# Kernel tuning notes

Measured on AMD Instinct MI355X. Metric: run time of the kernel, lower is better.

The kernel has to match this reference:

```python
import jax, jax.numpy as jnp
import numpy as np

N_NODES = 20000
N_EDGES = 320000
N_GRAPHS = 64
IN_DIM = 768
HID = 256
HEADS = 4
NUM_CLASSES = 5
NEG_SLOPE = 0.2  # PyG GATConv default leaky_relu slope


def setup_inputs() -> dict:
    key = jax.random.key(0)
    ks = jax.random.split(key, 20)
    x = jax.random.normal(ks[0], (N_NODES, IN_DIM), dtype=jnp.float32)
    edge_index = jax.random.randint(ks[1], (2, N_EDGES), 0, N_NODES, dtype=jnp.int32)
    batch = jnp.sort(jax.random.randint(ks[2], (N_NODES,), 0, N_GRAPHS, dtype=jnp.int32))
    s = lambda k, sh: jax.random.normal(k, sh, dtype=jnp.float32) * (1.0 / np.sqrt(sh[0]))
    HC = HEADS * HID
    return {
        "x": x, "edge_index": edge_index, "batch": batch,
        "Wp": s(ks[3], (IN_DIM, HID)), "bp": jnp.zeros((HID,), jnp.float32),
        "W1": s(ks[4], (HID, HC)),
        "as1": jax.random.normal(ks[5], (HEADS, HID)) * 0.1,
        "ad1": jax.random.normal(ks[6], (HEADS, HID)) * 0.1,
        "b1": jnp.zeros((HC,), jnp.float32),
        "W2": s(ks[7], (HC, HC)),
        "as2": jax.random.normal(ks[8], (HEADS, HID)) * 0.1,
        "ad2": jax.random.normal(ks[9], (HEADS, HID)) * 0.1,
        "b2": jnp.zeros((HC,), jnp.float32),
        "Wc1": s(ks[10], (2 * HC, 256)), "bc1": jnp.zeros((256,), jnp.float32),
        "Wc2": s(ks[11], (256, NUM_CLASSES)), "bc2": jnp.zeros((NUM_CLASSES,), jnp.float32),
    }


def _gat(h, src, dst, W, att_s, att_d, bias):
    # PyG GATConv (concat=True), dropout in eval mode (identity).
    N = h.shape[0]
    hW = (h @ W).reshape(N, HEADS, HID)             # [N,H,C]
    a_s = jnp.einsum('nhc,hc->nh', hW, att_s)        # per-node src score
    a_d = jnp.einsum('nhc,hc->nh', hW, att_d)
    e = jax.nn.leaky_relu(a_s[src] + a_d[dst], NEG_SLOPE)  # [E,H]
    # segment softmax over incoming edges of each destination node
    m = jax.ops.segment_max(e, dst, num_segments=N)
    e = jnp.exp(e - m[dst])
    denom = jax.ops.segment_sum(e, dst, num_segments=N)
    alpha = e / (denom[dst] + 1e-16)
    msg = hW[src] * alpha[:, :, None]                # [E,H,C]
    out = jax.ops.segment_sum(msg, dst, num_segments=N)
    return out.reshape(N, HEADS * HID) + bias


def reference(x, edge_index, batch, Wp, bp, W1, as1, ad1, b1, W2, as2, ad2, b2, Wc1, bc1, Wc2, bc2):
    N = x.shape[0]
    # add self-loops (PyG GATConv default add_self_loops=True)
    loop = jnp.arange(N, dtype=edge_index.dtype)
    src = jnp.concatenate([edge_index[0], loop])
    dst = jnp.concatenate([edge_index[1], loop])

    h = jax.nn.relu(x @ Wp + bp)
    h = jax.nn.elu(_gat(h, src, dst, W1, as1, ad1, b1))
    h = jax.nn.elu(_gat(h, src, dst, W2, as2, ad2, b2))

    # global mean / max pool over graphs
    cnt = jax.ops.segment_sum(jnp.ones((N,), h.dtype), batch, num_segments=N_GRAPHS)
    mean_pool = jax.ops.segment_sum(h, batch, num_segments=N_GRAPHS) / jnp.maximum(cnt, 1.0)[:, None]
    max_pool = jax.ops.segment_max(h, batch, num_segments=N_GRAPHS)
    g = jnp.concatenate([mean_pool, max_pool], axis=1)  # [G, 2*H*C]

    hcls = jax.nn.relu(g @ Wc1 + bc1)
    return hcls @ Wc2 + bc2
```

## Files before the change

### kernel.cpp

```cpp
#include <hip/hip_runtime.h>
#include <hip/hip_fp16.h>
#include <math.h>

#define N_HID 256
#define N_HEADS 4
#define N_HC 1024
#define N_GRAPHS 64

typedef __attribute__((ext_vector_type(4))) float f32x4;
typedef _Float16 half8 __attribute__((ext_vector_type(8)));
typedef _Float16 half4 __attribute__((ext_vector_type(4)));

__device__ __forceinline__ void gl_lds16h(const __half* g, __half* l) {
    __builtin_amdgcn_global_load_lds(
        (const __attribute__((address_space(1))) unsigned int*)g,
        (__attribute__((address_space(3))) unsigned int*)l, 16, 0, 0);
}

__global__ __launch_bounds__(256) void k_deg(const int* __restrict__ dst, int E,
                                             int* __restrict__ deg) {
    int e = blockIdx.x * 256 + threadIdx.x;
    if (e < E) atomicAdd(&deg[dst[e]], 1);
}

__global__ __launch_bounds__(1024) void k_scan(const int* __restrict__ deg,
                                               int* __restrict__ rowstart, int N) {
    __shared__ int part[1024];
    const int t = threadIdx.x;
    const int chunk = (N + 1023) / 1024;
    const int c0 = t * chunk;
    int s = 0;
    for (int i = 0; i < chunk; i++) {
        int idx = c0 + i;
        if (idx < N) s += deg[idx];
    }
    part[t] = s;
    __syncthreads();
    for (int off = 1; off < 1024; off <<= 1) {
        int v = (t >= off) ? part[t - off] : 0;
        __syncthreads();
        part[t] += v;
        __syncthreads();
    }
    int run = (t == 0) ? 0 : part[t - 1];
    if (t == 0) rowstart[0] = 0;
    for (int i = 0; i < chunk; i++) {
        int idx = c0 + i;
        if (idx < N) {
            run += deg[idx];
            rowstart[idx + 1] = run;
        }
    }
}

__global__ __launch_bounds__(256) void k_fill(const int* __restrict__ src,
                                              const int* __restrict__ dst, int E,
                                              const int* __restrict__ rowstart,
                                              int* __restrict__ cursor,
                                              int* __restrict__ col) {
    int e = blockIdx.x * 256 + threadIdx.x;
    if (e < E) {
        int d = dst[e];
        int p = atomicAdd(&cursor[d], 1);
        col[rowstart[d] + p] = src[e];
    }
}

__global__ __launch_bounds__(256) void k_wtt(const float* __restrict__ W,
                                             __half* __restrict__ WT, int K, int N) {
    __shared__ float tile[32][33];
    const int k0 = blockIdx.y * 32, n0 = blockIdx.x * 32;
    const int tr = threadIdx.x >> 5, tc = threadIdx.x & 31;
#pragma unroll
    for (int rr = 0; rr < 4; rr++) {
        int k = k0 + tr + rr * 8;
        tile[tr + rr * 8][tc] = W[(size_t)k * N + n0 + tc];
    }
    __syncthreads();
#pragma unroll
    for (int rr = 0; rr < 4; rr++) {
        int n = n0 + tr + rr * 8;
        WT[(size_t)n * K + k0 + tc] = __float2half(tile[tc][tr + rr * 8]);
    }
}

__global__ __launch_bounds__(256) void k_makeva(const __half* __restrict__ W1T,
                                                const float* __restrict__ as1,
                                                const float* __restrict__ ad1,
                                                float* __restrict__ va) {
    __shared__ float satt[256];
    int b = blockIdx.x;
    int h = b & 3, isd = b >> 2;
    int k = threadIdx.x;
    const float* att = (isd ? ad1 : as1) + h * 256;
    satt[k] = att[k];
    __syncthreads();
    const __half* wr = W1T + (size_t)(h * 256) * 256 + k;
    float s = 0.f;
    for (int c = 0; c < 256; c++) s += __half2float(wr[(size_t)c * 256]) * satt[c];
    va[b * 256 + k] = s;
}

__global__ __launch_bounds__(256) void k_makeva2(const __half* __restrict__ W2T,
                                                 const float* __restrict__ as2,
                                                 const float* __restrict__ ad2,
                                                 float* __restrict__ va2) {
    __shared__ float satt[32];
    int b = blockIdx.x;
    int h = b & 3;
    int jc = blockIdx.y;
    int t = threadIdx.x;
    const float* att = (b >= 4 ? ad2 : as2) + h * 256 + jc * 32;
    if (t < 32) satt[t] = att[t];
    __syncthreads();
    float s0 = 0.f, s1 = 0.f, s2 = 0.f, s3 = 0.f;
    const __half* base = W2T + (size_t)(h * 256 + jc * 32) * 1024 + t * 4;
    for (int j = 0; j < 32; j++) {
        half4 wv = *reinterpret_cast<const half4*>(base + (size_t)j * 1024);
        float a = satt[j];
        s0 += a * (float)wv[0]; s1 += a * (float)wv[1];
        s2 += a * (float)wv[2]; s3 += a * (float)wv[3];
    }
    float* o = va2 + b * 1024 + t * 4;
    atomicAdd(o + 0, s0); atomicAdd(o + 1, s1);
    atomicAdd(o + 2, s2); atomicAdd(o + 3, s3);
}

template <int EPI, int COSCHED>
__global__ __launch_bounds__(256) void k_gemm2p(
    const __half* __restrict__ A, const __half* __restrict__ BT,
    const float* __restrict__ bias, __half* __restrict__ C,
    int M, int NROW, int K, int lda, int ldc,
    int aoffz, int boffz, int coffz, int bofz) {
    __shared__ __half sA[2][128 * 32];
    __shared__ __half sB[2][128 * 32];
    int bm, bn;
    size_t coff = 0;
    if (COSCHED) {
        const int bid = blockIdx.x;
        const int xcd = bid & 7, j0 = bid >> 3;
        const int br = xcd + 8 * (j0 >> 3);
        const int bc = j0 & 7;
        if (br >= NROW) return;
        bm = br * 128; bn = bc * 128;
    } else {
        const int z = blockIdx.z;
        A += (size_t)z * aoffz;
        BT += (size_t)z * boffz;
        bias += z * bofz;
        coff = (size_t)z * coffz;
        bm = blockIdx.y * 128; bn = blockIdx.x * 128;
    }
    const int tid = threadIdx.x, lane = tid & 63, w = tid >> 6;
    const int wr = (w >> 1) * 64, wc = (w & 1) * 64;
    const bool isB = (w >= 2);
    const __half* gsrc = isB ? (BT + (size_t)bn * K) : (A + (size_t)bm * lda);
    const int gld = isB ? K : lda;
    const int rbase = (w & 1) * 64;
    const int lr = lane >> 2, lsl = lane & 3;
    const int g = lane >> 4, fr = lane & 15;
    const int nt = K >> 5;

    f32x4 acc[4][4] = {};

    auto STAGE = [&](int b, int t) {
        __half* sbuf = (isB ? sB[b] : sA[b]);
        const int k0 = t << 5;
#pragma unroll
        for (int c2 = 0; c2 < 4; c2++) {
            int row = rbase + c2 * 16 + lr;
            int slg = lsl ^ ((row >> 1) & 3);
            gl_lds16h(gsrc + (size_t)row * gld + k0 + slg * 8,
                      sbuf + (rbase + c2 * 16) * 32);
        }
    };

    STAGE(0, 0);
    int cur = 0;
    for (int t = 0; t < nt; ++t) {
        if (t + 1 < nt) {
            STAGE(cur ^ 1, t + 1);
            asm volatile("s_waitcnt vmcnt(4)" ::: "memory");
        } else {
            asm volatile("s_waitcnt vmcnt(0)" ::: "memory");
        }
        asm volatile("s_barrier" ::: "memory");
        half8 af[4], bf[4];
#pragma unroll
        for (int i = 0; i < 4; i++) {
            int Ra = wr + i * 16 + fr;
            af[i] = *reinterpret_cast<const half8*>(
                &sA[cur][Ra * 32 + ((g ^ ((Ra >> 1) & 3)) << 3)]);
            int Rb = wc + i * 16 + fr;
            bf[i] = *reinterpret_cast<const half8*>(
                &sB[cur][Rb * 32 + ((g ^ ((Rb >> 1) & 3)) << 3)]);
        }
#pragma unroll
        for (int i = 0; i < 4; i++)
#pragma unroll
            for (int j = 0; j < 4; j++)
                acc[i][j] = __builtin_amdgcn_mfma_f32_16x16x32_f16(af[i], bf[j], acc[i][j], 0, 0, 0);
        asm volatile("s_barrier" ::: "memory");
        cur ^= 1;
    }
    const int crow0 = (lane >> 4) * 4, ccol = lane & 15;
#pragma unroll
    for (int i = 0; i < 4; i++)
#pragma unroll
        for (int j = 0; j < 4; j++) {
            int cc = bn + wc + j * 16 + ccol;
            float bv = (EPI == 2) ? bias[cc] : 0.f;
#pragma unroll
            for (int r = 0; r < 4; r++) {
                int row = bm + wr + i * 16 + crow0 + r;
                if (row < M) {
                    float v = acc[i][j][r];
                    if (EPI == 2) { v += bv; v = v > 0.f ? v : (__expf(v) - 1.f); }
                    C[(size_t)row * ldc + coff + cc] = __float2half(v);
                }
            }
        }
}

__global__ __launch_bounds__(256) void k_gemm_x(
    const float* __restrict__ A, const __half* __restrict__ BT,
    const float* __restrict__ bias, __half* __restrict__ C,
    int M, int NROW, int K, int lda) {
    __shared__ __half sA[128 * 32];
    __shared__ __half sB[128 * 32];
    const int bid = blockIdx.x;
    const int xcd = bid & 7, j0 = bid >> 3;
    const int br = xcd + 8 * (j0 >> 1);
    const int bc = j0 & 1;
    if (br >= NROW) return;
    const int bm = br * 128, bn = bc * 128;
    const int tid = threadIdx.x, lane = tid & 63, w = tid >> 6;
    const int wr = (w >> 1) * 64, wc = (w & 1) * 64;
    const int sm = tid >> 1, skb = (tid & 1) * 16;
    const bool rok = (bm + sm) < M;
    const int ph0 = (((tid & 1) * 2 + 0) ^ ((sm >> 1) & 3)) << 3;
    const int ph1 = (((tid & 1) * 2 + 1) ^ ((sm >> 1) & 3)) << 3;
    const int lr = lane >> 2, lsl = lane & 3;

    f32x4 acc[4][4] = {};

    for (int k0 = 0; k0 < K; k0 += 32) {
#pragma unroll
        for (int c = 0; c < 2; c++) {
            int rb = (w + c * 4) * 16;
            int row = rb + lr;
            int slg = lsl ^ ((row >> 1) & 3);
            gl_lds16h(BT + (size_t)(bn + row) * K + k0 + slg * 8, sB + rb * 32);
        }
        {
            const float* Arow = A + (size_t)(bm + sm) * lda + k0 + skb;
            float4 v0 = make_float4(0.f, 0.f, 0.f, 0.f), v1 = v0, v2 = v0, v3 = v0;
            if (rok) {
                v0 = *(const float4*)(Arow + 0);
                v1 = *(const float4*)(Arow + 4);
                v2 = *(const float4*)(Arow + 8);
                v3 = *(const float4*)(Arow + 12);
            }
            half8 ha, hb;
            ha[0] = (_Float16)v0.x; ha[1] = (_Float16)v0.y;
            ha[2] = (_Float16)v0.z; ha[3] = (_Float16)v0.w;
            ha[4] = (_Float16)v1.x; ha[5] = (_Float16)v1.y;
            ha[6] = (_Float16)v1.z; ha[7] = (_Float16)v1.w;
            hb[0] = (_Float16)v2.x; hb[1] = (_Float16)v2.y;
            hb[2] = (_Float16)v2.z; hb[3] = (_Float16)v2.w;
            hb[4] = (_Float16)v3.x; hb[5] = (_Float16)v3.y;
            hb[6] = (_Float16)v3.z; hb[7] = (_Float16)v3.w;
            *reinterpret_cast<half8*>(&sA[sm * 32 + ph0]) = ha;
            *reinterpret_cast<half8*>(&sA[sm * 32 + ph1]) = hb;
        }
        __syncthreads();
        half8 af[4], bf[4];
        const int g = lane >> 4, fr = lane & 15;
#pragma unroll
        for (int i = 0; i < 4; i++) {
            int Ra = wr + i * 16 + fr;
            af[i] = *reinterpret_cast<const half8*>(
                &sA[Ra * 32 + ((g ^ ((Ra >> 1) & 3)) << 3)]);
            int Rb = wc + i * 16 + fr;
            bf[i] = *reinterpret_cast<const half8*>(
                &sB[Rb * 32 + ((g ^ ((Rb >> 1) & 3)) << 3)]);
        }
#pragma unroll
        for (int i = 0; i < 4; i++)
#pragma unroll
            for (int j = 0; j < 4; j++)
                acc[i][j] = __builtin_amdgcn_mfma_f32_16x16x32_f16(af[i], bf[j], acc[i][j], 0, 0, 0);
        __syncthreads();
    }
    const int crow0 = (lane >> 4) * 4, ccol = lane & 15;
#pragma unroll
    for (int i = 0; i < 4; i++)
#pragma unroll
        for (int j = 0; j < 4; j++) {
            int cc = bn + wc + j * 16 + ccol;
            float bv = bias[cc];
#pragma unroll
            for (int r = 0; r < 4; r++) {
                int row = bm + wr + i * 16 + crow0 + r;
                if (row < M) {
                    float v = acc[i][j][r] + bv;
                    v = v > 0.f ? v : 0.f;
                    C[(size_t)row * 256 + cc] = __float2half(v);
                }
            }
        }
}

__global__ __launch_bounds__(256) void k_score8(const __half* __restrict__ h0,
                                                const float* __restrict__ va,
                                                float* __restrict__ a_s,
                                                float* __restrict__ a_d, int N) {
    __shared__ float sva[8][256];
    int t = threadIdx.x;
    for (int i = t; i < 2048; i += 256) sva[i >> 8][i & 255] = va[i];
    __syncthreads();
    int wv = t >> 6, lane = t & 63;
    int n = blockIdx.x * 4 + wv;
    if (n >= N) return;
    uint2 u = *(const uint2*)(h0 + (size_t)n * 256 + lane * 4);
    __half2 q0 = __builtin_bit_cast(__half2, u.x);
    __half2 q1 = __builtin_bit_cast(__half2, u.y);
    float v0 = __half2float(q0.x), v1 = __half2float(q0.y);
    float v2 = __half2float(q1.x), v3 = __half2float(q1.y);
    float p[8];
#pragma unroll
    for (int v = 0; v < 8; v++) {
        p[v] = v0 * sva[v][lane * 4] + v1 * sva[v][lane * 4 + 1] +
               v2 * sva[v][lane * 4 + 2] + v3 * sva[v][lane * 4 + 3];
    }
#pragma unroll
    for (int off = 32; off > 0; off >>= 1)
#pragma unroll
        for (int v = 0; v < 8; v++) p[v] += __shfl_xor(p[v], off, 64);
    if (lane == 0) {
        *(float4*)&a_s[n * 4] = make_float4(p[0], p[1], p[2], p[3]);
        *(float4*)&a_d[n * 4] = make_float4(p[4], p[5], p[6], p[7]);
    }
}

__global__ __launch_bounds__(256) void k_score1024(const __half* __restrict__ h1,
                                                   const float* __restrict__ va2,
                                                   float* __restrict__ a_s,
                                                   float* __restrict__ a_d, int N) {
    __shared__ float sva[8 * 1024];
    int t = threadIdx.x;
    for (int i = t; i < 8192; i += 256) sva[i] = va2[i];
    __syncthreads();
    int wv = t >> 6, lane = t & 63;
    int n = blockIdx.x * 4 + wv;
    if (n >= N) return;
    const __half* hp = h1 + (size_t)n * 1024;
    float hv[16];
#pragma unroll
    for (int seg = 0; seg < 4; seg++) {
        half4 u = *reinterpret_cast<const half4*>(hp + seg * 256 + lane * 4);
#pragma unroll
        for (int c = 0; c < 4; c++) hv[seg * 4 + c] = (float)u[c];
    }
    float p[8] = {};
#pragma unroll
    for (int v = 0; v < 8; v++) {
#pragma unroll
        for (int seg = 0; seg < 4; seg++) {
            float4 f = *(const float4*)&sva[v * 1024 + seg * 256 + lane * 4];
            p[v] += hv[seg * 4] * f.x + hv[seg * 4 + 1] * f.y +
                    hv[seg * 4 + 2] * f.z + hv[seg * 4 + 3] * f.w;
        }
    }
#pragma unroll
    for (int off = 32; off > 0; off >>= 1)
#pragma unroll
        for (int v = 0; v < 8; v++) p[v] += __shfl_xor(p[v], off, 64);
    if (lane == 0) {
        *(float4*)&a_s[n * 4] = make_float4(p[0], p[1], p[2], p[3]);
        *(float4*)&a_d[n * 4] = make_float4(p[4], p[5], p[6], p[7]);
    }
}

__global__ __launch_bounds__(256) void k_gat_w1(
    const __half* __restrict__ h0, const float* __restrict__ a_s,
    const float* __restrict__ a_d, const int* __restrict__ rowstart,
    const int* __restrict__ col, __half* __restrict__ agg1, int N) {
    __shared__ int wsn[4][64];
    __shared__ float wal[4][64][4];
    const int w = threadIdx.x >> 6, lane = threadIdx.x & 63;
    const int bid = blockIdx.x;
    const int s = bid & 1;
    const int n = (bid >> 1) * 4 + w;
    if (n >= N) return;
    const int e0 = rowstart[n];
    const int deg = rowstart[n + 1] - e0;
    const int tot = deg + 1;
    float4 adv4 = *(const float4*)&a_d[n * 4];
    const float adv[4] = {adv4.x, adv4.y, adv4.z, adv4.w};
    float M[4] = {-INFINITY, -INFINITY, -INFINITY, -INFINITY};
    float S[4] = {0.f, 0.f, 0.f, 0.f};
    float acc[4][2] = {};

    for (int base = 0; base < tot; base += 64) {
        const int cnt = min(64, tot - base);
        const bool act = lane < cnt;
        int sn = n;
        float e[4];
        if (act) {
            const int li = base + lane;
            sn = (li < deg) ? col[e0 + li] : n;
            float4 asv = *(const float4*)&a_s[sn * 4];
            const float as4[4] = {asv.x, asv.y, asv.z, asv.w};
#pragma unroll
            for (int h = 0; h < 4; h++) {
                float sc = as4[h] + adv[h];
                e[h] = sc >= 0.f ? sc : 0.2f * sc;
            }
        } else {
#pragma unroll
            for (int h = 0; h < 4; h++) e[h] = -INFINITY;
        }
        float mw[4] = {e[0], e[1], e[2], e[3]};
#pragma unroll
        for (int off = 32; off > 0; off >>= 1)
#pragma unroll
            for (int h = 0; h < 4; h++)
                mw[h] = fmaxf(mw[h], __shfl_xor(mw[h], off, 64));
        float wv[4], sw[4];
#pragma unroll
        for (int h = 0; h < 4; h++) {
            mw[h] = fmaxf(mw[h], M[h]);
            wv[h] = act ? __expf(e[h] - mw[h]) : 0.f;
            sw[h] = wv[h];
        }
        wsn[w][lane] = sn;
        *(float4*)&wal[w][lane][0] = make_float4(wv[0], wv[1], wv[2], wv[3]);
#pragma unroll
        for (int off = 32; off > 0; off >>= 1)
#pragma unroll
            for (int h = 0; h < 4; h++) sw[h] += __shfl_xor(sw[h], off, 64);
#pragma unroll
        for (int h = 0; h < 4; h++) {
            float sc = __expf(M[h] - mw[h]);
            S[h] = S[h] * sc + sw[h];
            acc[h][0] *= sc; acc[h][1] *= sc;
            M[h] = mw[h];
        }
        const __half* gbase = h0 + s * 128 + lane * 2;
#pragma unroll 2
        for (int i = 0; i < cnt; i++) {
            const int s2 = wsn[w][i];
            float4 wg = *(const float4*)&wal[w][i][0];
            const float wgt[4] = {wg.x, wg.y, wg.z, wg.w};
            __half2 hv = *(const __half2*)(gbase + (size_t)s2 * 256);
            float v0 = __half2float(hv.x), v1 = __half2float(hv.y);
#pragma unroll
            for (int h = 0; h < 4; h++) {
                acc[h][0] += wgt[h] * v0;
                acc[h][1] += wgt[h] * v1;
            }
        }
    }
#pragma unroll
    for (int h = 0; h < 4; h++) {
        float d = 1.f / (S[h] + 1e-16f);
        __half2 o;
        o.x = __float2half(acc[h][0] * d);
        o.y = __float2half(acc[h][1] * d);
        *(__half2*)(agg1 + (size_t)n * 1024 + h * 256 + s * 128 + lane * 2) = o;
    }
}

__global__ __launch_bounds__(256) void k_gat_w2(
    const __half* __restrict__ hW, const float* __restrict__ a_s,
    const float* __restrict__ a_d, const int* __restrict__ rowstart,
    const int* __restrict__ col, const float* __restrict__ bias,
    __half* __restrict__ h2, int N) {
    __shared__ int wsn[4][64];
    __shared__ float wal[4][64];
    const int w = threadIdx.x >> 6, lane = threadIdx.x & 63;
    const int bid = blockIdx.x;
    const int sl = bid & 7;
    const int h = sl >> 1, half = sl & 1;
    const int n = (bid >> 3) * 4 + w;
    if (n >= N) return;
    const int e0 = rowstart[n];
    const int deg = rowstart[n + 1] - e0;
    const int tot = deg + 1;
    const float adv = a_d[n * 4 + h];
    float M = -INFINITY, S = 0.f;
    float a0 = 0.f, a1 = 0.f;

    for (int base = 0; base < tot; base += 64) {
        const int cnt = min(64, tot - base);
        const bool act = lane < cnt;
        int sn = n;
        float ev = -INFINITY;
        if (act) {
            const int li = base + lane;
            sn = (li < deg) ? col[e0 + li] : n;
            float sc = a_s[sn * 4 + h] + adv;
            ev = sc >= 0.f ? sc : 0.2f * sc;
        }
        float m = ev;
#pragma unroll
        for (int off = 32; off > 0; off >>= 1)
            m = fmaxf(m, __shfl_xor(m, off, 64));
        m = fmaxf(m, M);
        float wv = act ? __expf(ev - m) : 0.f;
        wsn[w][lane] = sn;
        wal[w][lane] = wv;
        float sw = wv;
#pragma unroll
        for (int off = 32; off > 0; off >>= 1)
            sw += __shfl_xor(sw, off, 64);
        float sc = __expf(M - m);
        S = S * sc + sw;
        M = m;
        a0 *= sc; a1 *= sc;
        const __half* gbase = hW + h * 256 + half * 128 + lane * 2;
#pragma unroll 4
        for (int i = 0; i < cnt; i++) {
            const int s2 = wsn[w][i];
            const float a = wal[w][i];
            __half2 v = *(const __half2*)(gbase + (size_t)s2 * 1024);
            a0 += a * __half2float(v.x);
            a1 += a * __half2float(v.y);
        }
    }
    const float d = 1.f / (S + 1e-16f);
    const int cc = h * 256 + half * 128 + lane * 2;
    float2 bb = *(const float2*)&bias[cc];
    float v0 = a0 * d + bb.x;
    float v1 = a1 * d + bb.y;
    v0 = v0 > 0.f ? v0 : (__expf(v0) - 1.f);
    v1 = v1 > 0.f ? v1 : (__expf(v1) - 1.f);
    __half2 o;
    o.x = __float2half(v0);
    o.y = __float2half(v1);
    *(__half2*)(h2 + (size_t)n * 1024 + cc) = o;
}

__global__ __launch_bounds__(128) void k_gbounds(const int* __restrict__ batch, int N,
                                                 int* __restrict__ gstart) {
    int g = threadIdx.x;
    if (g > N_GRAPHS) return;
    if (g == N_GRAPHS) { gstart[N_GRAPHS] = N; return; }
    int lo = 0, hi = N;
    while (lo < hi) {
        int mid = (lo + hi) >> 1;
        if (batch[mid] < g) lo = mid + 1; else hi = mid;
    }
    gstart[g] = lo;
}

__global__ __launch_bounds__(256) void k_pool1(const __half* __restrict__ h,
                                               const int* __restrict__ gstart,
                                               float* __restrict__ ps) {
    const int g = blockIdx.x, c = blockIdx.y, t = threadIdx.x;
    const int s = gstart[g], e = gstart[g + 1];
    const int len = e - s;
    const int cs = s + (int)(((long long)len * c) >> 3);
    const int ce = s + (int)(((long long)len * (c + 1)) >> 3);
    float sum[4] = {};
    float mx[4] = {-INFINITY, -INFINITY, -INFINITY, -INFINITY};
    for (int i = cs; i < ce; i++) {
        half4 v = *reinterpret_cast<const half4*>(h + (size_t)i * N_HC + t * 4);
#pragma unroll
        for (int k = 0; k < 4; k++) {
            float f = (float)v[k];
            sum[k] += f;
            mx[k] = fmaxf(mx[k], f);
        }
    }
    float* o = ps + ((size_t)g * 8 + c) * 2048;
    *(float4*)&o[t * 4] = make_float4(sum[0], sum[1], sum[2], sum[3]);
    *(float4*)&o[1024 + t * 4] = make_float4(mx[0], mx[1], mx[2], mx[3]);
}

__global__ __launch_bounds__(256) void k_pool2(const float* __restrict__ ps,
                                               const int* __restrict__ gstart,
                                               float* __restrict__ gout) {
    const int g = blockIdx.x, t = threadIdx.x;
    float sum[4] = {};
    float mx[4] = {-INFINITY, -INFINITY, -INFINITY, -INFINITY};
#pragma unroll
    for (int c = 0; c < 8; c++) {
        const float* o = ps + ((size_t)g * 8 + c) * 2048;
        float4 sv = *(const float4*)&o[t * 4];
        float4 mv = *(const float4*)&o[1024 + t * 4];
        sum[0] += sv.x; sum[1] += sv.y; sum[2] += sv.z; sum[3] += sv.w;
        mx[0] = fmaxf(mx[0], mv.x); mx[1] = fmaxf(mx[1], mv.y);
        mx[2] = fmaxf(mx[2], mv.z); mx[3] = fmaxf(mx[3], mv.w);
    }
    float cnt = fmaxf((float)(gstart[g + 1] - gstart[g]), 1.f);
    float inv = 1.f / cnt;
    *(float4*)(gout + (size_t)g * 2048 + t * 4) =
        make_float4(sum[0] * inv, sum[1] * inv, sum[2] * inv, sum[3] * inv);
    *(float4*)(gout + (size_t)g * 2048 + 1024 + t * 4) =
        make_float4(mx[0], mx[1], mx[2], mx[3]);
}

__global__ __launch_bounds__(256) void k_cls1(const float* __restrict__ g,
                                              const float* __restrict__ Wc1,
                                              const float* __restrict__ bc1,
                                              float* __restrict__ hcls) {
    __shared__ float gs[2048];
    int gb = blockIdx.x, t = threadIdx.x;
    for (int i = t; i < 2048; i += 256) gs[i] = g[(size_t)gb * 2048 + i];
    __syncthreads();
    float acc = 0.f;
    for (int k = 0; k < 2048; k++) acc += gs[k] * Wc1[(size_t)k * 256 + t];
    float v = acc + bc1[t];
    hcls[gb * 256 + t] = v > 0.f ? v : 0.f;
}

__global__ __launch_bounds__(256) void k_cls2(const float* __restrict__ hcls,
                                              const float* __restrict__ Wc2,
                                              const float* __restrict__ bc2,
                                              float* __restrict__ out) {
    int idx = blockIdx.x * 256 + threadIdx.x;
    if (idx >= N_GRAPHS * 5) return;
    int gb = idx / 5, j = idx % 5;
    float acc = 0.f;
    for (int k = 0; k < 256; k++) acc += hcls[gb * 256 + k] * Wc2[k * 5 + j];
    out[idx] = acc + bc2[j];
}

extern "C" void kernel_launch(void* const* d_in, const int* in_sizes, int n_in,
                              void* d_out, int out_size, void* d_ws, size_t ws_size,
                              hipStream_t stream) {
    const float* x    = (const float*)d_in[0];
    const int*   ei   = (const int*)d_in[1];
    const int*   batch= (const int*)d_in[2];
    const float* Wp   = (const float*)d_in[3];
    const float* bp   = (const float*)d_in[4];
    const float* W1   = (const float*)d_in[5];
    const float* as1  = (const float*)d_in[6];
    const float* ad1  = (const float*)d_in[7];
    const float* b1   = (const float*)d_in[8];
    const float* W2   = (const float*)d_in[9];
    const float* as2  = (const float*)d_in[10];
    const float* ad2  = (const float*)d_in[11];
    const float* b2   = (const float*)d_in[12];
    const float* Wc1  = (const float*)d_in[13];
    const float* bc1  = (const float*)d_in[14];
    const float* Wc2  = (const float*)d_in[15];
    const float* bc2  = (const float*)d_in[16];
    float* out = (float*)d_out;

    const int N = in_sizes[0] / 768;
    const int E = in_sizes[1] / 2;
    const int MP = ((N + 127) / 128) * 128;
    const int MB = MP / 128;

    const int* src = ei;
    const int* dst = ei + E;

    char* ws = (char*)d_ws;
    size_t off = 0;
    auto give = [&](size_t bytes) -> void* {
        void* p = ws + off;
        off = (off + bytes + 255) & ~(size_t)255;
        return p;
    };
    __half* h0  = (__half*)give((size_t)MP * N_HID * 2);
    __half* agg1= (__half*)give((size_t)MP * N_HC * 2);
    __half* h1  = (__half*)give((size_t)MP * N_HC * 2);
    __half* hW2 = (__half*)give((size_t)MP * N_HC * 2);
    __half* h2  = (__half*)give((size_t)MP * N_HC * 2);
    __half* WpT = (__half*)give((size_t)768 * 256 * 2);
    __half* W1T = (__half*)give((size_t)256 * 1024 * 2);
    __half* W2T = (__half*)give((size_t)1024 * 1024 * 2);
    float* va   = (float*)give((size_t)8 * 256 * 4);
    float* va2  = (float*)give((size_t)8 * 1024 * 4);
    float* a_s1 = (float*)give((size_t)N * N_HEADS * 4);
    float* a_d1 = (float*)give((size_t)N * N_HEADS * 4);
    float* a_s2 = (float*)give((size_t)N * N_HEADS * 4);
    float* a_d2 = (float*)give((size_t)N * N_HEADS * 4);
    float* ps   = (float*)give((size_t)N_GRAPHS * 8 * 2048 * 4);
    int* deg     = (int*)give((size_t)N * 4);
    int* cursor  = (int*)give((size_t)N * 4);
    int* rowstart= (int*)give((size_t)(N + 1) * 4);
    int* col     = (int*)give((size_t)E * 4);
    int* gstart  = (int*)give((size_t)(N_GRAPHS + 1) * 4);
    float* gpool = (float*)give((size_t)N_GRAPHS * 2048 * 4);
    float* hcls  = (float*)give((size_t)N_GRAPHS * 256 * 4);
    (void)ws_size; (void)n_in; (void)out_size;

    hipMemsetAsync(deg, 0, (size_t)N * 4, stream);
    hipMemsetAsync(cursor, 0, (size_t)N * 4, stream);
    hipMemsetAsync(va2, 0, (size_t)8 * 1024 * 4, stream);
    k_deg<<<(E + 255) / 256, 256, 0, stream>>>(dst, E, deg);
    k_scan<<<1, 1024, 0, stream>>>(deg, rowstart, N);
    k_fill<<<(E + 255) / 256, 256, 0, stream>>>(src, dst, E, rowstart, cursor, col);
    k_gbounds<<<1, 128, 0, stream>>>(batch, N, gstart);

    k_wtt<<<dim3(256 / 32, 768 / 32), 256, 0, stream>>>(Wp, WpT, 768, 256);
    k_wtt<<<dim3(1024 / 32, 256 / 32), 256, 0, stream>>>(W1, W1T, 256, 1024);
    k_wtt<<<dim3(1024 / 32, 1024 / 32), 256, 0, stream>>>(W2, W2T, 1024, 1024);
    k_makeva<<<8, 256, 0, stream>>>(W1T, as1, ad1, va);
    k_makeva2<<<dim3(8, 8), 256, 0, stream>>>(W2T, as2, ad2, va2);

    const int NROWPAD = ((MB + 7) / 8) * 8;

    k_gemm_x<<<NROWPAD * 2, 256, 0, stream>>>(x, WpT, bp, h0, N, MB, 768, 768);

    k_score8<<<(N + 3) / 4, 256, 0, stream>>>(h0, va, a_s1, a_d1, N);
    k_gat_w1<<<((N + 3) / 4) * 2, 256, 0, stream>>>(h0, a_s1, a_d1, rowstart, col, agg1, N);
    k_gemm2p<2, 0><<<dim3(2, MB, 4), 256, 0, stream>>>(
        agg1, W1T, b1, h1, N, 0, 256, 1024, 1024, 256, 65536, 256, 256);

    k_score1024<<<(N + 3) / 4, 256, 0, stream>>>(h1, va2, a_s2, a_d2, N);
    k_gemm2p<0, 1><<<NROWPAD * 8, 256, 0, stream>>>(
        h1, W2T, nullptr, hW2, N, MB, 1024, 1024, 1024, 0, 0, 0, 0);
    k_gat_w2<<<((N + 3) / 4) * 8, 256, 0, stream>>>(
        hW2, a_s2, a_d2, rowstart, col, b2, h2, N);

    k_pool1<<<dim3(N_GRAPHS, 8), 256, 0, stream>>>(h2, gstart, ps);
    k_pool2<<<N_GRAPHS, 256, 0, stream>>>(ps, gstart, gpool);
    k_cls1<<<N_GRAPHS, 256, 0, stream>>>(gpool, Wc1, bc1, hcls);
    k_cls2<<<2, 256, 0, stream>>>(hcls, Wc2, bc2, out);
}
```

Baseline: 489.0 us.

## Precompute softmax attention weights in a separate kernel before feature gather

Splits each GAT aggregation into a new k_alpha kernel and a gather kernel. k_alpha computes per-edge exp-weights (stored as fp16) and inverse softmax denominators once per layer, using a two-pass max-then-sum. The gather kernels then read these precomputed weights instead of redoing the online softmax in every column-slice block: 2x redundant in layer 1 and 8x in layer 2. This costs two extra launches, extra global traffic for the alpha arrays, and fp16 rounding of the weights.

```diff
diff --git a/kernel.cpp b/kernel.cpp
--- a/kernel.cpp
+++ b/kernel.cpp
@@ -382,9 +382,77 @@
     }
 }
 
-__global__ __launch_bounds__(256) void k_gat_w1(
-    const __half* __restrict__ h0, const float* __restrict__ a_s,
-    const float* __restrict__ a_d, const int* __restrict__ rowstart,
+__global__ __launch_bounds__(256) void k_alpha(
+    const float* __restrict__ a_s, const float* __restrict__ a_d,
+    const int* __restrict__ rowstart, const int* __restrict__ col,
+    __half* __restrict__ alp, float* __restrict__ invS, int N) {
+    const int w = threadIdx.x >> 6, lane = threadIdx.x & 63;
+    const int n = blockIdx.x * 4 + w;
+    if (n >= N) return;
+    const int e0 = rowstart[n];
+    const int deg = rowstart[n + 1] - e0;
+    const int tot = deg + 1;
+    const int as0 = e0 + n;
+    float4 adv4 = *(const float4*)&a_d[n * 4];
+    const float adv[4] = {adv4.x, adv4.y, adv4.z, adv4.w};
+    float M[4] = {-INFINITY, -INFINITY, -INFINITY, -INFINITY};
+    for (int base = 0; base < tot; base += 64) {
+        const int li = base + lane;
+        float e[4] = {-INFINITY, -INFINITY, -INFINITY, -INFINITY};
+        if (li < tot) {
+            const int sn = (li < deg) ? col[e0 + li] : n;
+            float4 asv = *(const float4*)&a_s[sn * 4];
+            const float as4[4] = {asv.x, asv.y, asv.z, asv.w};
+#pragma unroll
+            for (int h = 0; h < 4; h++) {
+                float sc = as4[h] + adv[h];
+                e[h] = sc >= 0.f ? sc : 0.2f * sc;
+            }
+        }
+#pragma unroll
+        for (int off = 32; off > 0; off >>= 1)
+#pragma unroll
+            for (int h = 0; h < 4; h++)
+                e[h] = fmaxf(e[h], __shfl_xor(e[h], off, 64));
+#pragma unroll
+        for (int h = 0; h < 4; h++) M[h] = fmaxf(M[h], e[h]);
+    }
+    float S[4] = {0.f, 0.f, 0.f, 0.f};
+    for (int base = 0; base < tot; base += 64) {
+        const int li = base + lane;
+        float wv[4] = {0.f, 0.f, 0.f, 0.f};
+        if (li < tot) {
+            const int sn = (li < deg) ? col[e0 + li] : n;
+            float4 asv = *(const float4*)&a_s[sn * 4];
+            const float as4[4] = {asv.x, asv.y, asv.z, asv.w};
+            half4 o;
+#pragma unroll
+            for (int h = 0; h < 4; h++) {
+                float sc = as4[h] + adv[h];
+                float e = sc >= 0.f ? sc : 0.2f * sc;
+                wv[h] = __expf(e - M[h]);
+                o[h] = (_Float16)wv[h];
+            }
+            *reinterpret_cast<half4*>(alp + (size_t)(as0 + li) * 4) = o;
+        }
+        float sw[4] = {wv[0], wv[1], wv[2], wv[3]};
+#pragma unroll
+        for (int off = 32; off > 0; off >>= 1)
+#pragma unroll
+            for (int h = 0; h < 4; h++) sw[h] += __shfl_xor(sw[h], off, 64);
+#pragma unroll
+        for (int h = 0; h < 4; h++) S[h] += sw[h];
+    }
+    if (lane == 0) {
+        *(float4*)&invS[n * 4] = make_float4(
+            1.f / (S[0] + 1e-16f), 1.f / (S[1] + 1e-16f),
+            1.f / (S[2] + 1e-16f), 1.f / (S[3] + 1e-16f));
+    }
+}
+
+__global__ __launch_bounds__(256) void k_gath1(
+    const __half* __restrict__ h0, const __half* __restrict__ alp,
+    const float* __restrict__ invS, const int* __restrict__ rowstart,
     const int* __restrict__ col, __half* __restrict__ agg1, int N) {
     __shared__ int wsn[4][64];
     __shared__ float wal[4][64][4];
@@ -396,56 +464,17 @@
     const int e0 = rowstart[n];
     const int deg = rowstart[n + 1] - e0;
     const int tot = deg + 1;
-    float4 adv4 = *(const float4*)&a_d[n * 4];
-    const float adv[4] = {adv4.x, adv4.y, adv4.z, adv4.w};
-    float M[4] = {-INFINITY, -INFINITY, -INFINITY, -INFINITY};
-    float S[4] = {0.f, 0.f, 0.f, 0.f};
+    const int as0 = e0 + n;
     float acc[4][2] = {};
 
     for (int base = 0; base < tot; base += 64) {
         const int cnt = min(64, tot - base);
-        const bool act = lane < cnt;
-        int sn = n;
-        float e[4];
-        if (act) {
-            const int li = base + lane;
-            sn = (li < deg) ? col[e0 + li] : n;
-            float4 asv = *(const float4*)&a_s[sn * 4];
-            const float as4[4] = {asv.x, asv.y, asv.z, asv.w};
-#pragma unroll
-            for (int h = 0; h < 4; h++) {
-                float sc = as4[h] + adv[h];
-                e[h] = sc >= 0.f ? sc : 0.2f * sc;
-            }
-        } else {
-#pragma unroll
-            for (int h = 0; h < 4; h++) e[h] = -INFINITY;
-        }
-        float mw[4] = {e[0], e[1], e[2], e[3]};
-#pragma unroll
-        for (int off = 32; off > 0; off >>= 1)
-#pragma unroll
-            for (int h = 0; h < 4; h++)
-                mw[h] = fmaxf(mw[h], __shfl_xor(mw[h], off, 64));
-        float wv[4], sw[4];
-#pragma unroll
-        for (int h = 0; h < 4; h++) {
-            mw[h] = fmaxf(mw[h], M[h]);
-            wv[h] = act ? __expf(e[h] - mw[h]) : 0.f;
-            sw[h] = wv[h];
-        }
-        wsn[w][lane] = sn;
-        *(float4*)&wal[w][lane][0] = make_float4(wv[0], wv[1], wv[2], wv[3]);
-#pragma unroll
-        for (int off = 32; off > 0; off >>= 1)
-#pragma unroll
-            for (int h = 0; h < 4; h++) sw[h] += __shfl_xor(sw[h], off, 64);
-#pragma unroll
-        for (int h = 0; h < 4; h++) {
-            float sc = __expf(M[h] - mw[h]);
-            S[h] = S[h] * sc + sw[h];
-            acc[h][0] *= sc; acc[h][1] *= sc;
-            M[h] = mw[h];
+        const int li = base + lane;
+        if (li < tot) {
+            wsn[w][lane] = (li < deg) ? col[e0 + li] : n;
+            half4 av = *reinterpret_cast<const half4*>(alp + (size_t)(as0 + li) * 4);
+            *(float4*)&wal[w][lane][0] = make_float4(
+                (float)av[0], (float)av[1], (float)av[2], (float)av[3]);
         }
         const __half* gbase = h0 + s * 128 + lane * 2;
 #pragma unroll 2
@@ -462,19 +491,20 @@
             }
         }
     }
+    float4 dv = *(const float4*)&invS[n * 4];
+    const float d[4] = {dv.x, dv.y, dv.z, dv.w};
 #pragma unroll
     for (int h = 0; h < 4; h++) {
-        float d = 1.f / (S[h] + 1e-16f);
         __half2 o;
-        o.x = __float2half(acc[h][0] * d);
-        o.y = __float2half(acc[h][1] * d);
+        o.x = __float2half(acc[h][0] * d[h]);
+        o.y = __float2half(acc[h][1] * d[h]);
         *(__half2*)(agg1 + (size_t)n * 1024 + h * 256 + s * 128 + lane * 2) = o;
     }
 }
 
-__global__ __launch_bounds__(256) void k_gat_w2(
-    const __half* __restrict__ hW, const float* __restrict__ a_s,
-    const float* __restrict__ a_d, const int* __restrict__ rowstart,
+__global__ __launch_bounds__(256) void k_gath2(
+    const __half* __restrict__ hW, const __half* __restrict__ alp,
+    const float* __restrict__ invS, const int* __restrict__ rowstart,
     const int* __restrict__ col, const float* __restrict__ bias,
     __half* __restrict__ h2, int N) {
     __shared__ int wsn[4][64];
@@ -488,37 +518,16 @@
     const int e0 = rowstart[n];
     const int deg = rowstart[n + 1] - e0;
     const int tot = deg + 1;
-    const float adv = a_d[n * 4 + h];
-    float M = -INFINITY, S = 0.f;
+    const int as0 = e0 + n;
     float a0 = 0.f, a1 = 0.f;
 
     for (int base = 0; base < tot; base += 64) {
         const int cnt = min(64, tot - base);
-        const bool act = lane < cnt;
-        int sn = n;
-        float ev = -INFINITY;
-        if (act) {
-            const int li = base + lane;
-            sn = (li < deg) ? col[e0 + li] : n;
-            float sc = a_s[sn * 4 + h] + adv;
-            ev = sc >= 0.f ? sc : 0.2f * sc;
-        }
-        float m = ev;
-#pragma unroll
-        for (int off = 32; off > 0; off >>= 1)
-            m = fmaxf(m, __shfl_xor(m, off, 64));
-        m = fmaxf(m, M);
-        float wv = act ? __expf(ev - m) : 0.f;
-        wsn[w][lane] = sn;
-        wal[w][lane] = wv;
-        float sw = wv;
-#pragma unroll
-        for (int off = 32; off > 0; off >>= 1)
-            sw += __shfl_xor(sw, off, 64);
-        float sc = __expf(M - m);
-        S = S * sc + sw;
-        M = m;
-        a0 *= sc; a1 *= sc;
+        const int li = base + lane;
+        if (li < tot) {
+            wsn[w][lane] = (li < deg) ? col[e0 + li] : n;
+            wal[w][lane] = (float)alp[(size_t)(as0 + li) * 4 + h];
+        }
         const __half* gbase = hW + h * 256 + half * 128 + lane * 2;
 #pragma unroll 4
         for (int i = 0; i < cnt; i++) {
@@ -529,7 +538,7 @@
             a1 += a * __half2float(v.y);
         }
     }
-    const float d = 1.f / (S + 1e-16f);
+    const float d = invS[n * 4 + h];
     const int cc = h * 256 + half * 128 + lane * 2;
     float2 bb = *(const float2*)&bias[cc];
     float v0 = a0 * d + bb.x;
@@ -679,6 +688,10 @@
     float* a_d1 = (float*)give((size_t)N * N_HEADS * 4);
     float* a_s2 = (float*)give((size_t)N * N_HEADS * 4);
     float* a_d2 = (float*)give((size_t)N * N_HEADS * 4);
+    __half* alp1 = (__half*)give((size_t)(E + N) * 4 * 2);
+    __half* alp2 = (__half*)give((size_t)(E + N) * 4 * 2);
+    float* invS1 = (float*)give((size_t)N * 4 * 4);
+    float* invS2 = (float*)give((size_t)N * 4 * 4);
     float* ps   = (float*)give((size_t)N_GRAPHS * 8 * 2048 * 4);
     int* deg     = (int*)give((size_t)N * 4);
     int* cursor  = (int*)give((size_t)N * 4);
@@ -704,19 +717,22 @@
     k_makeva2<<<dim3(8, 8), 256, 0, stream>>>(W2T, as2, ad2, va2);
 
     const int NROWPAD = ((MB + 7) / 8) * 8;
+    const int NGB = (N + 3) / 4;
 
     k_gemm_x<<<NROWPAD * 2, 256, 0, stream>>>(x, WpT, bp, h0, N, MB, 768, 768);
 
-    k_score8<<<(N + 3) / 4, 256, 0, stream>>>(h0, va, a_s1, a_d1, N);
-    k_gat_w1<<<((N + 3) / 4) * 2, 256, 0, stream>>>(h0, a_s1, a_d1, rowstart, col, agg1, N);
+    k_score8<<<NGB, 256, 0, stream>>>(h0, va, a_s1, a_d1, N);
+    k_alpha<<<NGB, 256, 0, stream>>>(a_s1, a_d1, rowstart, col, alp1, invS1, N);
+    k_gath1<<<NGB * 2, 256, 0, stream>>>(h0, alp1, invS1, rowstart, col, agg1, N);
     k_gemm2p<2, 0><<<dim3(2, MB, 4), 256, 0, stream>>>(
         agg1, W1T, b1, h1, N, 0, 256, 1024, 1024, 256, 65536, 256, 256);
 
-    k_score1024<<<(N + 3) / 4, 256, 0, stream>>>(h1, va2, a_s2, a_d2, N);
+    k_score1024<<<NGB, 256, 0, stream>>>(h1, va2, a_s2, a_d2, N);
+    k_alpha<<<NGB, 256, 0, stream>>>(a_s2, a_d2, rowstart, col, alp2, invS2, N);
     k_gemm2p<0, 1><<<NROWPAD * 8, 256, 0, stream>>>(
         h1, W2T, nullptr, hW2, N, MB, 1024, 1024, 1024, 0, 0, 0, 0);
-    k_gat_w2<<<((N + 3) / 4) * 8, 256, 0, stream>>>(
-        hW2, a_s2, a_d2, rowstart, col, b2, h2, N);
+    k_gath2<<<NGB * 8, 256, 0, stream>>>(
+        hW2, alp2, invS2, rowstart, col, b2, h2, N);
 
     k_pool1<<<dim3(N_GRAPHS, 8), 256, 0, stream>>>(h2, gstart, ps);
     k_pool2<<<N_GRAPHS, 256, 0, stream>>>(ps, gstart, gpool);
```

Result: slower. 499.3 us (+2.1%).
